# Kernel optimization log

Hardware: AMD Instinct MI355X
Metric: run time of the kernel (lower is better)

The kernel has to match this reference:

```python
import jax, jax.numpy as jnp
import numpy as np

B, S, D = 2, 2048, 2048
H, KVH, HD = 16, 4, 128
NREP = H // KVH  # GQA repeat factor


def _rope(x, cos, sin):
    # x: [B,S,h,HD]; pairs (x[2k], x[2k+1]) form complex numbers
    xr = x[..., 0::2]
    xi = x[..., 1::2]
    cos = cos[None, :, None, :]  # [1,S,1,HD/2]
    sin = sin[None, :, None, :]
    out_r = xr * cos - xi * sin
    out_i = xr * sin + xi * cos
    return jnp.stack([out_r, out_i], axis=-1).reshape(x.shape)


def setup_inputs() -> dict:
    key = jax.random.key(0)
    ks = jax.random.split(key, 5)
    x = jax.random.normal(ks[0], (B, S, D), dtype=jnp.float32)
    # standard rotary frequencies
    inv_freq = 1.0 / (10000.0 ** (np.arange(0, HD, 2, dtype=np.float64) / HD))
    ang = np.outer(np.arange(S, dtype=np.float64), inv_freq)
    freqs_cos = jnp.asarray(np.cos(ang), dtype=jnp.float32)  # [S, HD/2]
    freqs_sin = jnp.asarray(np.sin(ang), dtype=jnp.float32)
    wq = jax.random.normal(ks[1], (D, H * HD), dtype=jnp.float32) * 0.02
    wk = jax.random.normal(ks[2], (D, KVH * HD), dtype=jnp.float32) * 0.02
    wv = jax.random.normal(ks[3], (D, KVH * HD), dtype=jnp.float32) * 0.02
    wo = jax.random.normal(ks[4], (H * HD, D), dtype=jnp.float32) * 0.02
    cache_k = jnp.zeros((B, S, KVH, HD), dtype=jnp.float32)
    cache_v = jnp.zeros((B, S, KVH, HD), dtype=jnp.float32)
    return {"x": x, "freqs_cos": freqs_cos, "freqs_sin": freqs_sin,
            "wq": wq, "wk": wk, "wv": wv, "wo": wo,
            "cache_k": cache_k, "cache_v": cache_v, "start_pos": 0}


def reference(x, freqs_cos, freqs_sin, wq, wk, wv, wo, cache_k, cache_v, start_pos):
    b, s, _ = x.shape
    xq = (x @ wq).reshape(b, s, H, HD)
    xk = (x @ wk).reshape(b, s, KVH, HD)
    xv = (x @ wv).reshape(b, s, KVH, HD)
    xq = _rope(xq, freqs_cos, freqs_sin)
    xk = _rope(xk, freqs_cos, freqs_sin)
    # KV cache update + slice (start_pos is a static Python int)
    ck = cache_k.at[:, start_pos:start_pos + s].set(xk)
    cv = cache_v.at[:, start_pos:start_pos + s].set(xv)
    keys = ck[:, :start_pos + s]    # [B,T,KVH,HD]
    vals = cv[:, :start_pos + s]
    # GQA without materializing repeat_kv: group query heads per kv head
    q = xq.reshape(b, s, KVH, NREP, HD)
    scores = jnp.einsum('bsknd,btkd->bknst', q, keys) / np.float32(np.sqrt(HD))
    probs = jax.nn.softmax(scores.astype(jnp.float32), axis=-1).astype(x.dtype)
    out = jnp.einsum('bknst,btkd->bsknd', probs, vals).reshape(b, s, H * HD)
    return out @ wo
```

## Files before the change

kernel.cpp:

```cpp
#include <hip/hip_runtime.h>
#include <stdint.h>
#include <stddef.h>

#define S_LEN  2048
#define NH     16
#define NKVH   4
#define HD_    128
#define DMODEL 2048
#define NQKV   3072
#define MROWS  4096

typedef __attribute__((ext_vector_type(8)))  __bf16 bf16x8;
typedef __attribute__((ext_vector_type(4)))  __bf16 bf16x4;
typedef __attribute__((ext_vector_type(4)))  float  f32x4;
typedef __attribute__((ext_vector_type(16))) float  f32x16;

#define MFMA16(a, b, c) __builtin_amdgcn_mfma_f32_16x16x32_bf16((a), (b), (c), 0, 0, 0)
#define MFMA32(a, b, c) __builtin_amdgcn_mfma_f32_32x32x16_bf16((a), (b), (c), 0, 0, 0)

__device__ __forceinline__ void gload16(const void* g, void* l) {
  __builtin_amdgcn_global_load_lds((const __attribute__((address_space(1))) void*)g,
                                   (__attribute__((address_space(3))) void*)l,
                                   16, 0, 0);
}

__device__ __forceinline__ uint32_t cvtpk(float lo, float hi) {
  uint32_t d;
  asm("v_cvt_pk_bf16_f32 %0, %1, %2" : "=v"(d) : "v"(lo), "v"(hi));
  return d;
}
__device__ __forceinline__ void pswap(uint32_t& a, uint32_t& b) {
  asm("s_nop 1\n\tv_permlane32_swap_b32 %0, %1" : "+v"(a), "+v"(b));
}
__device__ __forceinline__ float fast_exp2(float x) {
  float r;
  asm("v_exp_f32 %0, %1\n\ts_nop 0" : "=v"(r) : "v"(x));
  return r;
}

__global__ void prep_kernel(const float* __restrict__ x, __bf16* __restrict__ xb,
                            const float* __restrict__ wq, const float* __restrict__ wk,
                            const float* __restrict__ wv, const float* __restrict__ wo,
                            __bf16* __restrict__ wqkvT, __bf16* __restrict__ woT) {
  __shared__ float tile[64][65];
  const int bid = blockIdx.x;
  const int tid = threadIdx.x;
  if (bid < 8192) {
    size_t i = (size_t)bid * 256 + tid;
    const float4* xv = (const float4*)x;
    float4 v = xv[i];
    bf16x4 o;
    o[0] = (__bf16)v.x; o[1] = (__bf16)v.y; o[2] = (__bf16)v.z; o[3] = (__bf16)v.w;
    *(bf16x4*)(xb + i * 4) = o;
    return;
  }
  int b2 = bid - 8192;
  const float* W; __bf16* WT; int ldw, kx, ny;
  if (b2 < 1024)      { W = wq; WT = wqkvT;                        ldw = 2048; kx = b2 & 31; ny = b2 >> 5; }
  else if (b2 < 1280) { int t = b2 - 1024; W = wk; WT = wqkvT + (size_t)2048 * 2048; ldw = 512; kx = t & 31; ny = t >> 5; }
  else if (b2 < 1536) { int t = b2 - 1280; W = wv; WT = wqkvT + (size_t)2560 * 2048; ldw = 512; kx = t & 31; ny = t >> 5; }
  else                { int t = b2 - 1536; W = wo; WT = woT;       ldw = 2048; kx = t & 31; ny = t >> 5; }
  const int k0 = kx * 64, n0 = ny * 64;
#pragma unroll
  for (int r = 0; r < 16; ++r) {
    int idx = r * 256 + tid;
    int kr = idx >> 6, nc = idx & 63;
    tile[kr][nc] = W[(size_t)(k0 + kr) * ldw + n0 + nc];
  }
  __syncthreads();
#pragma unroll
  for (int r = 0; r < 16; ++r) {
    int idx = r * 256 + tid;
    int nr = idx >> 6, kc = idx & 63;
    WT[(size_t)(n0 + nr) * 2048 + k0 + kc] = (__bf16)tile[kc][nr];
  }
}

template <int OUT_F32, int DO_ROPE>
__global__ __launch_bounds__(256, 2) void gemm_kernel(
    const __bf16* __restrict__ A, int lda,
    const __bf16* __restrict__ Bt, int ldb,
    void* __restrict__ Cout, int ldc, int Kdim,
    const float* __restrict__ fc, const float* __restrict__ fs) {
  __shared__ __attribute__((aligned(16))) __bf16 As[128 * 64];
  __shared__ __attribute__((aligned(16))) __bf16 Bs[128 * 64];
  const int tid = threadIdx.x;
  const int w = tid >> 6, l = tid & 63, lg = l >> 4, lr = l & 15;
  const int wm = w >> 1, wn = w & 1;
  const int m0 = blockIdx.y * 128, n0 = blockIdx.x * 128;

  f32x4 acc[4][4] = {};

  for (int k0 = 0; k0 < Kdim; k0 += 64) {
#pragma unroll
    for (int t = 0; t < 4; ++t) {
      int o = (t * 256 + tid) * 16;
      int row = o >> 7;
      int slot = (o >> 4) & 7;
      int sw = slot ^ (row & 7);
      gload16(A + (size_t)(m0 + row) * lda + k0 + sw * 8,
              (char*)As + t * 4096 + (w << 10));
      gload16(Bt + (size_t)(n0 + row) * ldb + k0 + sw * 8,
              (char*)Bs + t * 4096 + (w << 10));
    }
    __syncthreads();
#pragma unroll
    for (int c = 0; c < 2; ++c) {
      bf16x8 af[4];
#pragma unroll
      for (int mi = 0; mi < 4; ++mi) {
        int row = wm * 64 + mi * 16 + lr;
        int slot = (c * 4 + lg) ^ (row & 7);
        af[mi] = *(const bf16x8*)((const char*)As + row * 128 + slot * 16);
      }
#pragma unroll
      for (int ni = 0; ni < 4; ++ni) {
        int rn = wn * 64 + ni * 16 + lr;
        int slot = (c * 4 + lg) ^ (rn & 7);
        bf16x8 bfr = *(const bf16x8*)((const char*)Bs + rn * 128 + slot * 16);
#pragma unroll
        for (int mi = 0; mi < 4; ++mi)
          acc[mi][ni] = MFMA16(af[mi], bfr, acc[mi][ni]);
      }
    }
    __syncthreads();
  }

  if (DO_ROPE && n0 < 2560) {
    const float qs = 0.12755102871936672f;
#pragma unroll
    for (int mi = 0; mi < 4; ++mi)
#pragma unroll
      for (int ni = 0; ni < 4; ++ni)
#pragma unroll
        for (int i = 0; i < 4; ++i) {
          float v = acc[mi][ni][i];
          float p = __shfl_xor(v, 1);
          int cc = n0 + wn * 64 + ni * 16 + lr;
          int r  = m0 + wm * 64 + mi * 16 + lg * 4 + i;
          int s  = r & (S_LEN - 1);
          int j  = (cc & 127) >> 1;
          float c = fc[s * 64 + j], sn = fs[s * 64 + j];
          float o = (lr & 1) ? (p * sn + v * c)
                             : (v * c - p * sn);
          if (cc < DMODEL) o *= qs;
          ((__bf16*)Cout)[(size_t)r * ldc + cc] = (__bf16)o;
        }
    return;
  }

#pragma unroll
  for (int mi = 0; mi < 4; ++mi)
#pragma unroll
    for (int ni = 0; ni < 4; ++ni)
#pragma unroll
      for (int i = 0; i < 4; ++i) {
        int r = m0 + wm * 64 + mi * 16 + lg * 4 + i;
        int cc = n0 + wn * 64 + ni * 16 + lr;
        if (OUT_F32)
          ((float*)Cout)[(size_t)r * ldc + cc] = acc[mi][ni][i];
        else
          ((__bf16*)Cout)[(size_t)r * ldc + cc] = (__bf16)acc[mi][ni][i];
      }
}

__global__ void vt_kernel(const __bf16* __restrict__ qkv, __bf16* __restrict__ VT) {
  __shared__ uint16_t tile[64][66];
  const int bkv = blockIdx.z;
  const int b = bkv >> 2, kv = bkv & 3;
  const int s0 = blockIdx.x * 64, d0 = blockIdx.y * 64;
  const int tid = threadIdx.x;
#pragma unroll
  for (int r = 0; r < 16; ++r) {
    int idx = r * 256 + tid;
    int sr = idx >> 6, dc = idx & 63;
    tile[sr][dc] = *(const uint16_t*)(qkv + (size_t)(b * S_LEN + s0 + sr) * NQKV +
                                      (DMODEL + NKVH * HD_) + kv * HD_ + d0 + dc);
  }
  __syncthreads();
#pragma unroll
  for (int r = 0; r < 16; ++r) {
    int idx = r * 256 + tid;
    int dr = idx >> 6, sc = idx & 63;
    *(uint16_t*)(VT + (size_t)(bkv * HD_ + d0 + dr) * S_LEN + s0 + sc) = tile[sc][dr];
  }
}

__global__ __launch_bounds__(256, 2) void attn_kernel(
    const __bf16* __restrict__ qkv, const __bf16* __restrict__ VT,
    __bf16* __restrict__ out) {
  __shared__ __attribute__((aligned(16))) __bf16 Ks0[64 * 128];
  __shared__ __attribute__((aligned(16))) __bf16 Ks1[64 * 128];
  __shared__ __attribute__((aligned(16))) __bf16 Vs0[128 * 64];
  __shared__ __attribute__((aligned(16))) __bf16 Vs1[128 * 64];
  const int tid = threadIdx.x;
  const int w = tid >> 6, l = tid & 63;
  const int qc = l & 31, hi = l >> 5;
  const int bh = blockIdx.y;
  const int b = bh >> 4, h = bh & 15, kvh = h >> 2;
  const int q0 = blockIdx.x * 128 + w * 32;

  const __bf16* Kbase = qkv + (size_t)b * S_LEN * NQKV + DMODEL + kvh * HD_;
  const __bf16* Vbase = VT + (size_t)(b * NKVH + kvh) * (HD_ * S_LEN);

  auto stage = [&](int kt, __bf16* ksb, __bf16* vsb) {
#pragma unroll
    for (int t = 0; t < 4; ++t) {
      int o = (t * 256 + tid) * 16;
      {
        int row = o >> 8; int slot = (o >> 4) & 15; int sw = slot ^ (row & 7);
        gload16(Kbase + (size_t)(kt * 64 + row) * NQKV + sw * 8,
                (char*)ksb + t * 4096 + (w << 10));
      }
      {
        int row = o >> 7; int slot = (o >> 4) & 7; int sw = slot ^ (row & 7);
        gload16(Vbase + (size_t)row * S_LEN + kt * 64 + sw * 8,
                (char*)vsb + t * 4096 + (w << 10));
      }
    }
  };

  bf16x8 aq[8];
#pragma unroll
  for (int c = 0; c < 8; ++c)
    aq[c] = *(const bf16x8*)(qkv + (size_t)(b * S_LEN + q0 + qc) * NQKV +
                             h * HD_ + c * 16 + hi * 8);

  f32x16 o_acc[4] = {};
  float m = -1e30f, lsum = 0.0f;

  typedef union { uint32_t u[4]; bf16x8 v; } pfrag_t;

  auto tile_step = [&](const __bf16* ksb, const __bf16* vsb) {
    f32x16 st[2] = {};
    __builtin_amdgcn_s_setprio(1);
#pragma unroll
    for (int t = 0; t < 2; ++t) {
#pragma unroll
      for (int c = 0; c < 8; ++c) {
        int row = t * 32 + qc;
        int slot = (c * 2 + hi) ^ (row & 7);
        bf16x8 kf = *(const bf16x8*)((const char*)ksb + row * 256 + slot * 16);
        st[t] = MFMA32(kf, aq[c], st[t]);
      }
    }
    __builtin_amdgcn_s_setprio(0);

    float pm = st[0][0];
#pragma unroll
    for (int t = 0; t < 2; ++t)
#pragma unroll
      for (int r = 0; r < 16; ++r) pm = fmaxf(pm, st[t][r]);
    pm = fmaxf(pm, __shfl_xor(pm, 32));

    if (__any(pm - m > 11.54f)) {
      float mn = fmaxf(m, pm);
      float sf = fast_exp2(m - mn);
      lsum *= sf;
#pragma unroll
      for (int dt = 0; dt < 4; ++dt)
#pragma unroll
        for (int r = 0; r < 16; ++r) o_acc[dt][r] *= sf;
      m = mn;
    }

    float rsum = 0.0f;
#pragma unroll
    for (int t = 0; t < 2; ++t)
#pragma unroll
      for (int r = 0; r < 16; ++r) {
        st[t][r] = fast_exp2(st[t][r] - m);
        rsum += st[t][r];
      }
    rsum += __shfl_xor(rsum, 32);
    lsum += rsum;

    pfrag_t pf[4];
#pragma unroll
    for (int t = 0; t < 2; ++t)
#pragma unroll
      for (int half = 0; half < 2; ++half) {
        int bs = half * 8;
        uint32_t x0 = cvtpk(st[t][bs + 0], st[t][bs + 1]);
        uint32_t y0 = cvtpk(st[t][bs + 4], st[t][bs + 5]);
        uint32_t x1 = cvtpk(st[t][bs + 2], st[t][bs + 3]);
        uint32_t y1 = cvtpk(st[t][bs + 6], st[t][bs + 7]);
        pswap(x0, y0);
        pswap(x1, y1);
        pf[t * 2 + half].u[0] = x0;
        pf[t * 2 + half].u[1] = x1;
        pf[t * 2 + half].u[2] = y0;
        pf[t * 2 + half].u[3] = y1;
      }

    __builtin_amdgcn_s_setprio(1);
#pragma unroll
    for (int dt = 0; dt < 4; ++dt) {
#pragma unroll
      for (int ks = 0; ks < 4; ++ks) {
        int row = dt * 32 + qc;
        int slot = (ks * 2 + hi) ^ (row & 7);
        bf16x8 vf = *(const bf16x8*)((const char*)vsb + row * 128 + slot * 16);
        o_acc[dt] = MFMA32(vf, pf[ks].v, o_acc[dt]);
      }
    }
    __builtin_amdgcn_s_setprio(0);
  };

  stage(0, Ks0, Vs0);
  __syncthreads();

#pragma unroll 1
  for (int kt = 0; kt < S_LEN / 64; kt += 2) {
    stage(kt + 1, Ks1, Vs1);
    tile_step(Ks0, Vs0);
    __syncthreads();
    if (kt + 2 < S_LEN / 64) stage(kt + 2, Ks0, Vs0);
    tile_step(Ks1, Vs1);
    __syncthreads();
  }

  float rinv = 1.0f / lsum;
  const size_t orow = (size_t)(b * S_LEN + q0 + qc) * DMODEL + h * HD_;
#pragma unroll
  for (int dt = 0; dt < 4; ++dt)
#pragma unroll
    for (int rg = 0; rg < 4; ++rg) {
      bf16x4 ov;
#pragma unroll
      for (int i = 0; i < 4; ++i)
        ov[i] = (__bf16)(o_acc[dt][rg * 4 + i] * rinv);
      int d = dt * 32 + rg * 8 + hi * 4;
      *(bf16x4*)(out + orow + d) = ov;
    }
}

extern "C" void kernel_launch(void* const* d_in, const int* in_sizes, int n_in,
                              void* d_out, int out_size, void* d_ws, size_t ws_size,
                              hipStream_t stream) {
  const float* x  = (const float*)d_in[0];
  const float* fc = (const float*)d_in[1];
  const float* fs = (const float*)d_in[2];
  const float* wq = (const float*)d_in[3];
  const float* wk = (const float*)d_in[4];
  const float* wv = (const float*)d_in[5];
  const float* wo = (const float*)d_in[6];

  char* ws = (char*)d_ws;
  __bf16* xb    = (__bf16*)(ws);
  __bf16* wqkvT = (__bf16*)(ws + (16u << 20));
  __bf16* woT   = (__bf16*)(ws + (28u << 20));
  __bf16* qkv   = (__bf16*)(ws + (36u << 20));
  __bf16* VT    = (__bf16*)(ws + (60u << 20));

  prep_kernel<<<10752, 256, 0, stream>>>(x, xb, wq, wk, wv, wo, wqkvT, woT);
  {
    dim3 g(NQKV / 128, MROWS / 128);
    gemm_kernel<0, 1><<<g, 256, 0, stream>>>(xb, 2048, wqkvT, 2048, qkv, NQKV, 2048, fc, fs);
  }
  {
    dim3 g(32, 2, 8); vt_kernel<<<g, 256, 0, stream>>>(qkv, VT);
  }
  {
    dim3 g(S_LEN / 128, 32); attn_kernel<<<g, 256, 0, stream>>>(qkv, VT, xb);
  }
  {
    dim3 g(DMODEL / 128, MROWS / 128);
    gemm_kernel<1, 0><<<g, 256, 0, stream>>>(xb, 2048, woT, 2048, d_out, 2048, 2048, fc, fs);
  }
}
```

Baseline: 193.9 us.

## Write K and V in pre-tiled attention layout from QKV GEMM epilogue

The QKV GEMM epilogue now writes Q to its own buffer and scatters K and the transposed V straight into a tile-contiguous layout matching the attention kernel's LDS fragment order. This removes the separate V-transpose kernel launch and its extra global traffic. It also turns attention staging into plain contiguous 16-byte loads with simple LDS addressing. In exchange, the epilogue stores become scattered 2-byte writes with poor coalescing, and the unswizzled LDS layout may cause bank conflicts.

```diff
diff --git a/kernel.cpp b/kernel.cpp
--- a/kernel.cpp
+++ b/kernel.cpp
@@ -76,12 +76,13 @@
   }
 }
 
-template <int OUT_F32, int DO_ROPE>
+template <int MODE>
 __global__ __launch_bounds__(256, 2) void gemm_kernel(
     const __bf16* __restrict__ A, int lda,
     const __bf16* __restrict__ Bt, int ldb,
     void* __restrict__ Cout, int ldc, int Kdim,
-    const float* __restrict__ fc, const float* __restrict__ fs) {
+    const float* __restrict__ fc, const float* __restrict__ fs,
+    __bf16* __restrict__ xq, __bf16* __restrict__ Kp, __bf16* __restrict__ VTp) {
   __shared__ __attribute__((aligned(16))) __bf16 As[128 * 64];
   __shared__ __attribute__((aligned(16))) __bf16 Bs[128 * 64];
   const int tid = threadIdx.x;
@@ -126,26 +127,52 @@
     __syncthreads();
   }
 
-  if (DO_ROPE && n0 < 2560) {
+  if (MODE == 1) {
     const float qs = 0.12755102871936672f;
-#pragma unroll
-    for (int mi = 0; mi < 4; ++mi)
-#pragma unroll
-      for (int ni = 0; ni < 4; ++ni)
-#pragma unroll
-        for (int i = 0; i < 4; ++i) {
-          float v = acc[mi][ni][i];
-          float p = __shfl_xor(v, 1);
-          int cc = n0 + wn * 64 + ni * 16 + lr;
-          int r  = m0 + wm * 64 + mi * 16 + lg * 4 + i;
-          int s  = r & (S_LEN - 1);
-          int j  = (cc & 127) >> 1;
-          float c = fc[s * 64 + j], sn = fs[s * 64 + j];
-          float o = (lr & 1) ? (p * sn + v * c)
-                             : (v * c - p * sn);
-          if (cc < DMODEL) o *= qs;
-          ((__bf16*)Cout)[(size_t)r * ldc + cc] = (__bf16)o;
-        }
+    if (n0 < 2560) {
+#pragma unroll
+      for (int mi = 0; mi < 4; ++mi)
+#pragma unroll
+        for (int ni = 0; ni < 4; ++ni)
+#pragma unroll
+          for (int i = 0; i < 4; ++i) {
+            float v = acc[mi][ni][i];
+            float p = __shfl_xor(v, 1);
+            int cc = n0 + wn * 64 + ni * 16 + lr;
+            int r  = m0 + wm * 64 + mi * 16 + lg * 4 + i;
+            int s  = r & (S_LEN - 1);
+            int j  = (cc & 127) >> 1;
+            float c = fc[s * 64 + j], sn = fs[s * 64 + j];
+            float o = (lr & 1) ? (p * sn + v * c)
+                               : (v * c - p * sn);
+            if (n0 < DMODEL) {
+              xq[(size_t)r * DMODEL + cc] = (__bf16)(o * qs);
+            } else {
+              int bb = r >> 11, kt = s >> 6, rr = s & 63;
+              int kvh = (cc - DMODEL) >> 7, dk = (cc - DMODEL) & 127;
+              size_t e = ((size_t)((bb * 4 + kvh) * 32 + kt) * 16 + (dk >> 3)) * 512
+                         + rr * 8 + (dk & 7);
+              Kp[e] = (__bf16)o;
+            }
+          }
+    } else {
+#pragma unroll
+      for (int mi = 0; mi < 4; ++mi)
+#pragma unroll
+        for (int ni = 0; ni < 4; ++ni)
+#pragma unroll
+          for (int i = 0; i < 4; ++i) {
+            float v = acc[mi][ni][i];
+            int cc = n0 + wn * 64 + ni * 16 + lr;
+            int r  = m0 + wm * 64 + mi * 16 + lg * 4 + i;
+            int s  = r & (S_LEN - 1);
+            int bb = r >> 11, kt = s >> 6, rr = s & 63;
+            int kvh = (cc - 2560) >> 7, d = (cc - 2560) & 127;
+            size_t e = ((size_t)((bb * 4 + kvh) * 32 + kt) * 8 + (rr >> 3)) * 1024
+                       + d * 8 + (rr & 7);
+            VTp[e] = (__bf16)v;
+          }
+    }
     return;
   }
 
@@ -157,38 +184,13 @@
       for (int i = 0; i < 4; ++i) {
         int r = m0 + wm * 64 + mi * 16 + lg * 4 + i;
         int cc = n0 + wn * 64 + ni * 16 + lr;
-        if (OUT_F32)
-          ((float*)Cout)[(size_t)r * ldc + cc] = acc[mi][ni][i];
-        else
-          ((__bf16*)Cout)[(size_t)r * ldc + cc] = (__bf16)acc[mi][ni][i];
-      }
-}
-
-__global__ void vt_kernel(const __bf16* __restrict__ qkv, __bf16* __restrict__ VT) {
-  __shared__ uint16_t tile[64][66];
-  const int bkv = blockIdx.z;
-  const int b = bkv >> 2, kv = bkv & 3;
-  const int s0 = blockIdx.x * 64, d0 = blockIdx.y * 64;
-  const int tid = threadIdx.x;
-#pragma unroll
-  for (int r = 0; r < 16; ++r) {
-    int idx = r * 256 + tid;
-    int sr = idx >> 6, dc = idx & 63;
-    tile[sr][dc] = *(const uint16_t*)(qkv + (size_t)(b * S_LEN + s0 + sr) * NQKV +
-                                      (DMODEL + NKVH * HD_) + kv * HD_ + d0 + dc);
-  }
-  __syncthreads();
-#pragma unroll
-  for (int r = 0; r < 16; ++r) {
-    int idx = r * 256 + tid;
-    int dr = idx >> 6, sc = idx & 63;
-    *(uint16_t*)(VT + (size_t)(bkv * HD_ + d0 + dr) * S_LEN + s0 + sc) = tile[sc][dr];
-  }
+        ((float*)Cout)[(size_t)r * ldc + cc] = acc[mi][ni][i];
+      }
 }
 
 __global__ __launch_bounds__(256, 2) void attn_kernel(
-    const __bf16* __restrict__ qkv, const __bf16* __restrict__ VT,
-    __bf16* __restrict__ out) {
+    const __bf16* __restrict__ xq, const __bf16* __restrict__ Kp,
+    const __bf16* __restrict__ VTp, __bf16* __restrict__ out) {
   __shared__ __attribute__((aligned(16))) __bf16 Ks0[64 * 128];
   __shared__ __attribute__((aligned(16))) __bf16 Ks1[64 * 128];
   __shared__ __attribute__((aligned(16))) __bf16 Vs0[128 * 64];
@@ -198,32 +200,26 @@
   const int qc = l & 31, hi = l >> 5;
   const int bh = blockIdx.y;
   const int b = bh >> 4, h = bh & 15, kvh = h >> 2;
+  const int bkv = b * NKVH + kvh;
   const int q0 = blockIdx.x * 128 + w * 32;
 
-  const __bf16* Kbase = qkv + (size_t)b * S_LEN * NQKV + DMODEL + kvh * HD_;
-  const __bf16* Vbase = VT + (size_t)(b * NKVH + kvh) * (HD_ * S_LEN);
+  const __bf16* Ktiles = Kp  + (size_t)bkv * 32 * 8192;
+  const __bf16* Vtiles = VTp + (size_t)bkv * 32 * 8192;
 
   auto stage = [&](int kt, __bf16* ksb, __bf16* vsb) {
+    const __bf16* ksrc = Ktiles + (size_t)kt * 8192;
+    const __bf16* vsrc = Vtiles + (size_t)kt * 8192;
 #pragma unroll
     for (int t = 0; t < 4; ++t) {
-      int o = (t * 256 + tid) * 16;
-      {
-        int row = o >> 8; int slot = (o >> 4) & 15; int sw = slot ^ (row & 7);
-        gload16(Kbase + (size_t)(kt * 64 + row) * NQKV + sw * 8,
-                (char*)ksb + t * 4096 + (w << 10));
-      }
-      {
-        int row = o >> 7; int slot = (o >> 4) & 7; int sw = slot ^ (row & 7);
-        gload16(Vbase + (size_t)row * S_LEN + kt * 64 + sw * 8,
-                (char*)vsb + t * 4096 + (w << 10));
-      }
+      gload16(ksrc + (t * 256 + tid) * 8, (char*)ksb + t * 4096 + (w << 10));
+      gload16(vsrc + (t * 256 + tid) * 8, (char*)vsb + t * 4096 + (w << 10));
     }
   };
 
   bf16x8 aq[8];
 #pragma unroll
   for (int c = 0; c < 8; ++c)
-    aq[c] = *(const bf16x8*)(qkv + (size_t)(b * S_LEN + q0 + qc) * NQKV +
+    aq[c] = *(const bf16x8*)(xq + (size_t)(b * S_LEN + q0 + qc) * DMODEL +
                              h * HD_ + c * 16 + hi * 8);
 
   f32x16 o_acc[4] = {};
@@ -232,15 +228,16 @@
   typedef union { uint32_t u[4]; bf16x8 v; } pfrag_t;
 
   auto tile_step = [&](const __bf16* ksb, const __bf16* vsb) {
+    const char* kb = (const char*)ksb + hi * 1024 + qc * 16;
+    const char* vb = (const char*)vsb + hi * 2048 + qc * 16;
+
     f32x16 st[2] = {};
     __builtin_amdgcn_s_setprio(1);
 #pragma unroll
     for (int t = 0; t < 2; ++t) {
 #pragma unroll
       for (int c = 0; c < 8; ++c) {
-        int row = t * 32 + qc;
-        int slot = (c * 2 + hi) ^ (row & 7);
-        bf16x8 kf = *(const bf16x8*)((const char*)ksb + row * 256 + slot * 16);
+        bf16x8 kf = *(const bf16x8*)(kb + c * 2048 + t * 512);
         st[t] = MFMA32(kf, aq[c], st[t]);
       }
     }
@@ -298,9 +295,7 @@
     for (int dt = 0; dt < 4; ++dt) {
 #pragma unroll
       for (int ks = 0; ks < 4; ++ks) {
-        int row = dt * 32 + qc;
-        int slot = (ks * 2 + hi) ^ (row & 7);
-        bf16x8 vf = *(const bf16x8*)((const char*)vsb + row * 128 + slot * 16);
+        bf16x8 vf = *(const bf16x8*)(vb + ks * 4096 + dt * 512);
         o_acc[dt] = MFMA32(vf, pf[ks].v, o_acc[dt]);
       }
     }
@@ -350,22 +345,23 @@
   __bf16* xb    = (__bf16*)(ws);
   __bf16* wqkvT = (__bf16*)(ws + (16u << 20));
   __bf16* woT   = (__bf16*)(ws + (28u << 20));
-  __bf16* qkv   = (__bf16*)(ws + (36u << 20));
-  __bf16* VT    = (__bf16*)(ws + (60u << 20));
+  __bf16* xq    = (__bf16*)(ws + (36u << 20));
+  __bf16* Kp    = (__bf16*)(ws + (52u << 20));
+  __bf16* VTp   = (__bf16*)(ws + (56u << 20));
 
   prep_kernel<<<10752, 256, 0, stream>>>(x, xb, wq, wk, wv, wo, wqkvT, woT);
   {
     dim3 g(NQKV / 128, MROWS / 128);
-    gemm_kernel<0, 1><<<g, 256, 0, stream>>>(xb, 2048, wqkvT, 2048, qkv, NQKV, 2048, fc, fs);
+    gemm_kernel<1><<<g, 256, 0, stream>>>(xb, 2048, wqkvT, 2048, nullptr, 0, 2048,
+                                          fc, fs, xq, Kp, VTp);
   }
   {
-    dim3 g(32, 2, 8); vt_kernel<<<g, 256, 0, stream>>>(qkv, VT);
-  }
-  {
-    dim3 g(S_LEN / 128, 32); attn_kernel<<<g, 256, 0, stream>>>(qkv, VT, xb);
+    dim3 g(S_LEN / 128, 32);
+    attn_kernel<<<g, 256, 0, stream>>>(xq, Kp, VTp, xb);
   }
   {
     dim3 g(DMODEL / 128, MROWS / 128);
-    gemm_kernel<1, 0><<<g, 256, 0, stream>>>(xb, 2048, woT, 2048, d_out, 2048, 2048, fc, fs);
-  }
-}
+    gemm_kernel<0><<<g, 256, 0, stream>>>(xb, 2048, woT, 2048, d_out, 2048, 2048,
+                                          fc, fs, nullptr, nullptr, nullptr);
+  }
+}
```

New measurement: 194.4 us. No clear change (+0.3%).
